# Performance work log

Hardware: AMD Instinct MI355X
Metric: run time of the kernel (lower is better)

Reference implementation:

```python
import jax, jax.numpy as jnp
import numpy as np

DIM = 96          # channels (= groups for depthwise conv)
NUM_EXPERTS = 6
TOP_K = 3
B, H, W = 8, 192, 192


def _dwconv(x, w, b):
    # depthwise 3x3, stride 1, pad 1, groups = DIM (flag == 'C' branch)
    y = jax.lax.conv_general_dilated(
        x, w, window_strides=(1, 1), padding=((1, 1), (1, 1)),
        feature_group_count=DIM,
        dimension_numbers=('NCHW', 'OIHW', 'NCHW'))
    return y + b[None, :, None, None]


def _expert(x, w1, b1, w2, b2):
    return _dwconv(jax.nn.relu(_dwconv(x, w1, b1)), w2, b2)


def _gate(x, w_fc0, b_fc0, w_fc1, b_fc1):
    # AdaptiveMaxPool2d(1) + AdaptiveAvgPool2d(1), then flatten -> (B, DIM)
    pooled = jnp.max(x, axis=(2, 3)) + jnp.mean(x, axis=(2, 3))
    g = jax.nn.leaky_relu(pooled @ w_fc1.T + b_fc1, negative_slope=0.2)
    noise = jax.nn.softplus(pooled @ w_fc0.T + b_fc0)
    mu = jnp.mean(noise, axis=1, keepdims=True)
    sd = jnp.std(noise, axis=1, keepdims=True, ddof=1)  # torch.std is unbiased
    scores = g + (noise - mu) / sd
    _, idx = jax.lax.top_k(scores, TOP_K)  # (B, K)
    mask = jnp.any(jax.nn.one_hot(idx, NUM_EXPERTS, dtype=jnp.float32) > 0, axis=1)  # (B, E)
    # non-top-k logits of g set to -inf, softmax over experts
    return jax.nn.softmax(jnp.where(mask, g, -jnp.inf), axis=1)


def setup_inputs() -> dict:
    key = jax.random.key(0)
    ks = jax.random.split(key, 9)
    s = 0.05
    return {
        'x': jax.random.normal(ks[0], (B, DIM, H, W), jnp.float32),
        'w_fc0': jax.random.normal(ks[1], (NUM_EXPERTS, DIM), jnp.float32) * s,
        'b_fc0': jax.random.normal(ks[2], (NUM_EXPERTS,), jnp.float32) * s,
        'w_fc1': jax.random.normal(ks[3], (NUM_EXPERTS, DIM), jnp.float32) * s,
        'b_fc1': jax.random.normal(ks[4], (NUM_EXPERTS,), jnp.float32) * s,
        'ew1': jax.random.normal(ks[5], (NUM_EXPERTS, DIM, 1, 3, 3), jnp.float32) * s,
        'eb1': jax.random.normal(ks[6], (NUM_EXPERTS, DIM), jnp.float32) * s,
        'ew2': jax.random.normal(ks[7], (NUM_EXPERTS, DIM, 1, 3, 3), jnp.float32) * s,
        'eb2': jax.random.normal(ks[8], (NUM_EXPERTS, DIM), jnp.float32) * s,
    }


def reference(x, w_fc0, b_fc0, w_fc1, b_fc1, ew1, eb1, ew2, eb2):
    cof = _gate(x, w_fc0, b_fc0, w_fc1, b_fc1)  # (B, E), zero for non-top-k
    # Dense dispatch: experts with cof==0 contribute nothing, matching the
    # torch masked gather/scatter-accumulate loop exactly.
    outs = jax.vmap(lambda w1, b1, w2, b2: _expert(x, w1, b1, w2, b2))(
        ew1, eb1, ew2, eb2)  # (E, B, C, H, W)
    return jnp.einsum('ebchw,be->bchw', outs, cof)
```

## Files before the change

### kernel.cpp

```cpp
#include <hip/hip_runtime.h>
#include <math.h>

#define DIM 96
#define NE 6
#define NB 8
#define H 192
#define W 192
#define HW (H * W)
#define NQ 4
#define QF4 (HW / 4 / NQ)

__global__ __launch_bounds__(256) void pool_partial(const float* __restrict__ x,
                                                    float* __restrict__ pmax,
                                                    float* __restrict__ psum) {
    int bc = blockIdx.x;
    int q = blockIdx.y;
    const float4* xp = (const float4*)(x + (size_t)bc * HW) + q * QF4;
    int tid = threadIdx.x;
    float vmax = -INFINITY, vsum = 0.f;
    for (int i = tid; i < QF4; i += 256) {
        float4 v = xp[i];
        vmax = fmaxf(vmax, fmaxf(fmaxf(v.x, v.y), fmaxf(v.z, v.w)));
        vsum += v.x + v.y + v.z + v.w;
    }
    for (int off = 32; off; off >>= 1) {
        vmax = fmaxf(vmax, __shfl_down(vmax, off, 64));
        vsum += __shfl_down(vsum, off, 64);
    }
    __shared__ float smax[4], ssum[4];
    if ((tid & 63) == 0) { smax[tid >> 6] = vmax; ssum[tid >> 6] = vsum; }
    __syncthreads();
    if (tid == 0) {
        float m = smax[0], s = ssum[0];
        for (int w = 1; w < 4; ++w) { m = fmaxf(m, smax[w]); s += ssum[w]; }
        pmax[q * (NB * DIM) + bc] = m;
        psum[q * (NB * DIM) + bc] = s;
    }
}

__global__ __launch_bounds__(128) void gate_kernel(const float* __restrict__ pmax,
                                                   const float* __restrict__ psum,
                                                   const float* __restrict__ w_fc0,
                                                   const float* __restrict__ b_fc0,
                                                   const float* __restrict__ w_fc1,
                                                   const float* __restrict__ b_fc1,
                                                   float* __restrict__ cof) {
    __shared__ float sp[NB * DIM];
    __shared__ float sw1[NE * DIM], sw0[NE * DIM];
    __shared__ float z1s[NB * NE], z0s[NB * NE];
    int tid = threadIdx.x;
    for (int i = tid; i < NB * DIM; i += 128) {
        float m = pmax[i], s = psum[i];
        for (int q = 1; q < NQ; ++q) {
            m = fmaxf(m, pmax[q * (NB * DIM) + i]);
            s += psum[q * (NB * DIM) + i];
        }
        sp[i] = m + s * (1.0f / (float)HW);
    }
    for (int i = tid; i < NE * DIM; i += 128) {
        sw1[i] = w_fc1[i];
        sw0[i] = w_fc0[i];
    }
    __syncthreads();
    if (tid < 2 * NB * NE) {
        int pair = (tid < NB * NE) ? tid : tid - NB * NE;
        int b = pair / NE, e = pair - b * NE;
        const float* wp = ((tid < NB * NE) ? sw1 : sw0) + e * DIM;
        float z = (tid < NB * NE) ? b_fc1[e] : b_fc0[e];
        const float* pp = sp + b * DIM;
        for (int i = 0; i < DIM; ++i) z = fmaf(pp[i], wp[i], z);
        if (tid < NB * NE) z1s[pair] = z; else z0s[pair] = z;
    }
    __syncthreads();
    if (tid < NB) {
        int b = tid;
        float g[NE], noise[NE];
        for (int e = 0; e < NE; ++e) {
            float z1 = z1s[b * NE + e], z0 = z0s[b * NE + e];
            g[e] = (z1 > 0.f) ? z1 : 0.2f * z1;
            noise[e] = (z0 > 20.f) ? z0 : log1pf(expf(z0));
        }
        float mu = 0.f;
        for (int e = 0; e < NE; ++e) mu += noise[e];
        mu *= (1.0f / NE);
        float var = 0.f;
        for (int e = 0; e < NE; ++e) { float d = noise[e] - mu; var += d * d; }
        var *= (1.0f / (NE - 1));
        float sd = sqrtf(var);
        float scores[NE];
        for (int e = 0; e < NE; ++e) scores[e] = g[e] + (noise[e] - mu) / sd;
        bool chosen[NE] = {false, false, false, false, false, false};
        for (int k = 0; k < 3; ++k) {
            float best = -INFINITY; int bi = 0;
            for (int e = 0; e < NE; ++e)
                if (!chosen[e] && scores[e] > best) { best = scores[e]; bi = e; }
            chosen[bi] = true;
        }
        float m = -INFINITY;
        for (int e = 0; e < NE; ++e) if (chosen[e]) m = fmaxf(m, g[e]);
        float s = 0.f;
        for (int e = 0; e < NE; ++e) if (chosen[e]) s += expf(g[e] - m);
        float inv = 1.0f / s;
        for (int e = 0; e < NE; ++e)
            cof[b * NE + e] = chosen[e] ? expf(g[e] - m) * inv : 0.f;
    }
}

#define TX 64
#define TY 32
#define IX (TX + 4)
#define IY (TY + 4)
#define YX (TX + 2)
#define YY (TY + 2)

__global__ __launch_bounds__(256) void moe_kernel(const float* __restrict__ x,
                                                  const float* __restrict__ ew1,
                                                  const float* __restrict__ eb1,
                                                  const float* __restrict__ ew2,
                                                  const float* __restrict__ eb2,
                                                  const float* __restrict__ cof,
                                                  float* __restrict__ out) {
    __shared__ float xs[IY][IX];
    __shared__ float ys[YY][YX];
    const int tile = blockIdx.x;
    const int c = blockIdx.y;
    const int b = blockIdx.z;
    const int tx0 = (tile % (W / TX)) * TX;
    const int ty0 = (tile / (W / TX)) * TY;
    const int tid = threadIdx.x;
    const int tx = tid & 63;
    const int wv = (tid >> 6) & 3;

    const float* xp = x + ((size_t)(b * DIM + c)) * HW;

    #pragma unroll
    for (int rr = 0; rr < 9; ++rr) {
        int r = wv + rr * 4;
        int gh = ty0 + r - 2;
        int gw = tx0 + tx - 2;
        float v = 0.f, v2 = 0.f;
        if (gh >= 0 && gh < H) {
            if (gw >= 0 && gw < W) v = xp[gh * W + gw];
            int gw2 = gw + 64;
            if (tx < 4 && gw2 < W) v2 = xp[gh * W + gw2];
        }
        xs[r][tx] = v;
        if (tx < 4) xs[r][tx + 64] = v2;
    }

    const bool topB = (ty0 == 0), botB = (ty0 == H - TY);
    const bool leftB = (tx0 == 0), rightB = (tx0 == W - TX);
    const int zr0 = topB ? 0 : -1;
    const int zr1 = botB ? (YY - 1) : -1;
    const bool lzero = leftB && (tx == 0);

    float acc[8];
    #pragma unroll
    for (int i = 0; i < 8; ++i) acc[i] = 0.f;

    const int rs = wv * 8 + (wv ? 1 : 0);
    const int r2 = wv * 8;

    for (int e = 0; e < NE; ++e) {
        float ce = cof[b * NE + e];
        if (ce == 0.f) continue;
        const float* w1 = ew1 + (size_t)(e * DIM + c) * 9;
        const float* w2 = ew2 + (size_t)(e * DIM + c) * 9;
        float w1r[9], w2r[9];
        #pragma unroll
        for (int k = 0; k < 9; ++k) { w1r[k] = w1[k]; w2r[k] = w2[k]; }
        const float bb1 = eb1[e * DIM + c];
        const float bb2 = eb2[e * DIM + c];

        __syncthreads();

        {
            float a0 = xs[rs][tx], a1 = xs[rs][tx + 1], a2 = xs[rs][tx + 2];
            float b0 = xs[rs + 1][tx], b1 = xs[rs + 1][tx + 1], b2 = xs[rs + 1][tx + 2];
            #pragma unroll
            for (int j = 0; j < 9; ++j) {
                int r = rs + j;
                float c0 = xs[r + 2][tx], c1 = xs[r + 2][tx + 1], c2 = xs[r + 2][tx + 2];
                float s = fmaf(w1r[0], a0, fmaf(w1r[1], a1, fmaf(w1r[2], a2, bb1)));
                s = fmaf(w1r[3], b0, fmaf(w1r[4], b1, fmaf(w1r[5], b2, s)));
                s = fmaf(w1r[6], c0, fmaf(w1r[7], c1, fmaf(w1r[8], c2, s)));
                float v = fmaxf(s, 0.f);
                if (r == zr0 || r == zr1 || lzero) v = 0.f;
                ys[r][tx] = v;
                a0 = b0; a1 = b1; a2 = b2;
                b0 = c0; b1 = c1; b2 = c2;
            }
        }
        if (tid < 2 * YY) {
            int r = tid >> 1;
            int cc = 64 + (tid & 1);
            float s = bb1;
            #pragma unroll
            for (int dr = 0; dr < 3; ++dr)
                #pragma unroll
                for (int dc = 0; dc < 3; ++dc)
                    s = fmaf(w1r[dr * 3 + dc], xs[r + dr][cc + dc], s);
            float v = fmaxf(s, 0.f);
            if (r == zr0 || r == zr1 || (rightB && cc == YX - 1)) v = 0.f;
            ys[r][cc] = v;
        }
        __syncthreads();

        {
            float p0 = ys[r2][tx], p1 = ys[r2][tx + 1], p2 = ys[r2][tx + 2];
            float q0 = ys[r2 + 1][tx], q1 = ys[r2 + 1][tx + 1], q2 = ys[r2 + 1][tx + 2];
            #pragma unroll
            for (int j = 0; j < 8; ++j) {
                float u0 = ys[r2 + j + 2][tx], u1 = ys[r2 + j + 2][tx + 1], u2 = ys[r2 + j + 2][tx + 2];
                float s = fmaf(w2r[0], p0, fmaf(w2r[1], p1, fmaf(w2r[2], p2, bb2)));
                s = fmaf(w2r[3], q0, fmaf(w2r[4], q1, fmaf(w2r[5], q2, s)));
                s = fmaf(w2r[6], u0, fmaf(w2r[7], u1, fmaf(w2r[8], u2, s)));
                acc[j] = fmaf(ce, s, acc[j]);
                p0 = q0; p1 = q1; p2 = q2;
                q0 = u0; q1 = u1; q2 = u2;
            }
        }
    }

    float* op = out + ((size_t)(b * DIM + c)) * HW + (size_t)(ty0 + r2) * W + tx0 + tx;
    #pragma unroll
    for (int j = 0; j < 8; ++j) op[j * W] = acc[j];
}

extern "C" void kernel_launch(void* const* d_in, const int* in_sizes, int n_in,
                              void* d_out, int out_size, void* d_ws, size_t ws_size,
                              hipStream_t stream) {
    const float* x     = (const float*)d_in[0];
    const float* w_fc0 = (const float*)d_in[1];
    const float* b_fc0 = (const float*)d_in[2];
    const float* w_fc1 = (const float*)d_in[3];
    const float* b_fc1 = (const float*)d_in[4];
    const float* ew1   = (const float*)d_in[5];
    const float* eb1   = (const float*)d_in[6];
    const float* ew2   = (const float*)d_in[7];
    const float* eb2   = (const float*)d_in[8];
    float* out = (float*)d_out;

    float* pmax = (float*)d_ws;
    float* psum = pmax + NQ * NB * DIM;
    float* cof  = psum + NQ * NB * DIM;

    dim3 pg(NB * DIM, NQ);
    pool_partial<<<pg, 256, 0, stream>>>(x, pmax, psum);
    gate_kernel<<<1, 128, 0, stream>>>(pmax, psum, w_fc0, b_fc0, w_fc1, b_fc1, cof);
    dim3 grid((W / TX) * (H / TY), DIM, NB);
    moe_kernel<<<grid, 256, 0, stream>>>(x, ew1, eb1, ew2, eb2, cof, out);
}
```

Before: 279.9 us.

## Restructure expert conv into full-width row strips with register-resident intermediates

The MoE kernel now has each block own a full-width 32-row strip. Each lane computes 3 adjacent columns and keeps the first conv's ReLU output in registers, trading neighbour values with wave shuffles instead of a shared-memory intermediate tile and its barriers. The three selected experts are found once up front, made wave-uniform with readfirstlane, and processed together per row, so the input is loaded into shared memory once with float4 reads. This removes repeated LDS round-trips and per-expert syncs and cuts halo recomputation, at the cost of much higher register pressure (weights for three experts plus rolling row buffers) and strided 3-element global stores.

```diff
diff --git a/kernel.cpp b/kernel.cpp
--- a/kernel.cpp
+++ b/kernel.cpp
@@ -106,12 +106,25 @@
     }
 }
 
-#define TX 64
 #define TY 32
-#define IX (TX + 4)
-#define IY (TY + 4)
-#define YX (TX + 2)
-#define YY (TY + 2)
+#define RPW 8
+#define SW 200
+#define XROWS (TY + 4)
+
+__device__ __forceinline__ float c3(const float* Wt, float bb,
+                                    const float* A, const float* B,
+                                    const float* Cc, int o) {
+    float s = fmaf(Wt[2], A[o + 2], bb);
+    s = fmaf(Wt[1], A[o + 1], s);
+    s = fmaf(Wt[0], A[o], s);
+    s = fmaf(Wt[5], B[o + 2], s);
+    s = fmaf(Wt[4], B[o + 1], s);
+    s = fmaf(Wt[3], B[o], s);
+    s = fmaf(Wt[8], Cc[o + 2], s);
+    s = fmaf(Wt[7], Cc[o + 1], s);
+    s = fmaf(Wt[6], Cc[o], s);
+    return s;
+}
 
 __global__ __launch_bounds__(256) void moe_kernel(const float* __restrict__ x,
                                                   const float* __restrict__ ew1,
@@ -120,111 +133,129 @@
                                                   const float* __restrict__ eb2,
                                                   const float* __restrict__ cof,
                                                   float* __restrict__ out) {
-    __shared__ float xs[IY][IX];
-    __shared__ float ys[YY][YX];
-    const int tile = blockIdx.x;
+    __shared__ float xs[XROWS * SW];
+    const int sb = blockIdx.x;
     const int c = blockIdx.y;
     const int b = blockIdx.z;
-    const int tx0 = (tile % (W / TX)) * TX;
-    const int ty0 = (tile / (W / TX)) * TY;
+    const int ty0 = sb * TY;
     const int tid = threadIdx.x;
-    const int tx = tid & 63;
-    const int wv = (tid >> 6) & 3;
+    const int lane = tid & 63;
+    const int wv = tid >> 6;
+
+    if (tid < 2 * XROWS) {
+        int r = tid >> 1;
+        int side = tid & 1;
+        *(float4*)&xs[r * SW + side * 196] = make_float4(0.f, 0.f, 0.f, 0.f);
+    }
 
     const float* xp = x + ((size_t)(b * DIM + c)) * HW;
-
-    #pragma unroll
-    for (int rr = 0; rr < 9; ++rr) {
-        int r = wv + rr * 4;
-        int gh = ty0 + r - 2;
-        int gw = tx0 + tx - 2;
-        float v = 0.f, v2 = 0.f;
-        if (gh >= 0 && gh < H) {
-            if (gw >= 0 && gw < W) v = xp[gh * W + gw];
-            int gw2 = gw + 64;
-            if (tx < 4 && gw2 < W) v2 = xp[gh * W + gw2];
-        }
-        xs[r][tx] = v;
-        if (tx < 4) xs[r][tx + 64] = v2;
-    }
-
-    const bool topB = (ty0 == 0), botB = (ty0 == H - TY);
-    const bool leftB = (tx0 == 0), rightB = (tx0 == W - TX);
-    const int zr0 = topB ? 0 : -1;
-    const int zr1 = botB ? (YY - 1) : -1;
-    const bool lzero = leftB && (tx == 0);
-
-    float acc[8];
-    #pragma unroll
-    for (int i = 0; i < 8; ++i) acc[i] = 0.f;
-
-    const int rs = wv * 8 + (wv ? 1 : 0);
-    const int r2 = wv * 8;
-
+    #pragma unroll
+    for (int it = 0; it < 7; ++it) {
+        int f = tid + it * 256;
+        if (f < XROWS * 48) {
+            int r = f / 48;
+            int k = f - r * 48;
+            int gh = ty0 + r - 2;
+            float4 v = make_float4(0.f, 0.f, 0.f, 0.f);
+            if (gh >= 0 && gh < H) v = *(const float4*)(xp + (size_t)gh * W + k * 4);
+            *(float4*)&xs[r * SW + 4 + k * 4] = v;
+        }
+    }
+
+    const float* cofb = cof + b * NE;
+    int e0 = 0, e1 = 0, e2 = 0;
+    float q0 = 0.f, q1 = 0.f, q2 = 0.f;
+    int n = 0;
+    #pragma unroll
     for (int e = 0; e < NE; ++e) {
-        float ce = cof[b * NE + e];
-        if (ce == 0.f) continue;
-        const float* w1 = ew1 + (size_t)(e * DIM + c) * 9;
-        const float* w2 = ew2 + (size_t)(e * DIM + c) * 9;
-        float w1r[9], w2r[9];
+        float ce = cofb[e];
+        if (ce != 0.f) {
+            if (n == 0)      { e0 = e; q0 = ce; }
+            else if (n == 1) { e1 = e; q1 = ce; }
+            else if (n == 2) { e2 = e; q2 = ce; }
+            ++n;
+        }
+    }
+    e0 = __builtin_amdgcn_readfirstlane(e0);
+    e1 = __builtin_amdgcn_readfirstlane(e1);
+    e2 = __builtin_amdgcn_readfirstlane(e2);
+    q0 = __int_as_float(__builtin_amdgcn_readfirstlane(__float_as_int(q0)));
+    q1 = __int_as_float(__builtin_amdgcn_readfirstlane(__float_as_int(q1)));
+    q2 = __int_as_float(__builtin_amdgcn_readfirstlane(__float_as_int(q2)));
+
+    const int eidx[3] = { e0, e1, e2 };
+    const float qv[3] = { q0, q1, q2 };
+    float W1[3][9], W2[3][9], B1[3], B2[3], CE[3];
+    #pragma unroll
+    for (int t = 0; t < 3; ++t) {
+        const int e = eidx[t];
+        const float* p1 = ew1 + (size_t)(e * DIM + c) * 9;
+        const float* p2 = ew2 + (size_t)(e * DIM + c) * 9;
         #pragma unroll
-        for (int k = 0; k < 9; ++k) { w1r[k] = w1[k]; w2r[k] = w2[k]; }
-        const float bb1 = eb1[e * DIM + c];
-        const float bb2 = eb2[e * DIM + c];
-
-        __syncthreads();
-
-        {
-            float a0 = xs[rs][tx], a1 = xs[rs][tx + 1], a2 = xs[rs][tx + 2];
-            float b0 = xs[rs + 1][tx], b1 = xs[rs + 1][tx + 1], b2 = xs[rs + 1][tx + 2];
-            #pragma unroll
-            for (int j = 0; j < 9; ++j) {
-                int r = rs + j;
-                float c0 = xs[r + 2][tx], c1 = xs[r + 2][tx + 1], c2 = xs[r + 2][tx + 2];
-                float s = fmaf(w1r[0], a0, fmaf(w1r[1], a1, fmaf(w1r[2], a2, bb1)));
-                s = fmaf(w1r[3], b0, fmaf(w1r[4], b1, fmaf(w1r[5], b2, s)));
-                s = fmaf(w1r[6], c0, fmaf(w1r[7], c1, fmaf(w1r[8], c2, s)));
-                float v = fmaxf(s, 0.f);
-                if (r == zr0 || r == zr1 || lzero) v = 0.f;
-                ys[r][tx] = v;
-                a0 = b0; a1 = b1; a2 = b2;
-                b0 = c0; b1 = c1; b2 = c2;
+        for (int k = 0; k < 9; ++k) { W1[t][k] = p1[k]; W2[t][k] = p2[k]; }
+        B1[t] = eb1[e * DIM + c];
+        B2[t] = eb2[e * DIM + c];
+        CE[t] = qv[t];
+    }
+
+    __syncthreads();
+
+    const int r0 = ty0 + wv * RPW;
+    const int lbase = (wv * RPW) * SW + 3 * lane + 3;
+    const bool l0 = (lane == 0);
+    const bool l63 = (lane == 63);
+
+    float X[3][5];
+    float Y[3][3][5];
+    #pragma unroll
+    for (int k = 0; k < 5; ++k) X[0][k] = xs[lbase + k];
+    #pragma unroll
+    for (int k = 0; k < 5; ++k) X[1][k] = xs[lbase + SW + k];
+
+    float* op = out + ((size_t)(b * DIM + c)) * HW + (size_t)r0 * W + 3 * lane;
+
+    #pragma unroll
+    for (int j = 0; j < RPW + 2; ++j) {
+        float* xN = X[(j + 2) % 3];
+        #pragma unroll
+        for (int k = 0; k < 5; ++k) xN[k] = xs[lbase + (j + 2) * SW + k];
+        const float* xA = X[j % 3];
+        const float* xB = X[(j + 1) % 3];
+        const float* xC = xN;
+        float a0 = 0.f, a1 = 0.f, a2 = 0.f;
+        #pragma unroll
+        for (int t = 0; t < 3; ++t) {
+            float y0 = c3(W1[t], B1[t], xA, xB, xC, 0);
+            float y1 = c3(W1[t], B1[t], xA, xB, xC, 1);
+            float y2 = c3(W1[t], B1[t], xA, xB, xC, 2);
+            y0 = fmaxf(y0, 0.f); y1 = fmaxf(y1, 0.f); y2 = fmaxf(y2, 0.f);
+            if (j == 0 || j == RPW + 1) {
+                int ry = r0 - 1 + j;
+                if (ry < 0 || ry >= H) { y0 = 0.f; y1 = 0.f; y2 = 0.f; }
             }
-        }
-        if (tid < 2 * YY) {
-            int r = tid >> 1;
-            int cc = 64 + (tid & 1);
-            float s = bb1;
-            #pragma unroll
-            for (int dr = 0; dr < 3; ++dr)
-                #pragma unroll
-                for (int dc = 0; dc < 3; ++dc)
-                    s = fmaf(w1r[dr * 3 + dc], xs[r + dr][cc + dc], s);
-            float v = fmaxf(s, 0.f);
-            if (r == zr0 || r == zr1 || (rightB && cc == YX - 1)) v = 0.f;
-            ys[r][cc] = v;
-        }
-        __syncthreads();
-
-        {
-            float p0 = ys[r2][tx], p1 = ys[r2][tx + 1], p2 = ys[r2][tx + 2];
-            float q0 = ys[r2 + 1][tx], q1 = ys[r2 + 1][tx + 1], q2 = ys[r2 + 1][tx + 2];
-            #pragma unroll
-            for (int j = 0; j < 8; ++j) {
-                float u0 = ys[r2 + j + 2][tx], u1 = ys[r2 + j + 2][tx + 1], u2 = ys[r2 + j + 2][tx + 2];
-                float s = fmaf(w2r[0], p0, fmaf(w2r[1], p1, fmaf(w2r[2], p2, bb2)));
-                s = fmaf(w2r[3], q0, fmaf(w2r[4], q1, fmaf(w2r[5], q2, s)));
-                s = fmaf(w2r[6], u0, fmaf(w2r[7], u1, fmaf(w2r[8], u2, s)));
-                acc[j] = fmaf(ce, s, acc[j]);
-                p0 = q0; p1 = q1; p2 = q2;
-                q0 = u0; q1 = u1; q2 = u2;
+            float yl = __shfl_up(y2, 1);
+            float yr = __shfl_down(y0, 1);
+            if (l0) yl = 0.f;
+            if (l63) yr = 0.f;
+            float* yw = Y[t][j % 3];
+            yw[0] = yl; yw[1] = y0; yw[2] = y1; yw[3] = y2; yw[4] = yr;
+            if (j >= 2) {
+                const float* pA = Y[t][(j + 1) % 3];
+                const float* pB = Y[t][(j + 2) % 3];
+                const float* pC = yw;
+                float s0 = c3(W2[t], B2[t], pA, pB, pC, 0);
+                float s1 = c3(W2[t], B2[t], pA, pB, pC, 1);
+                float s2 = c3(W2[t], B2[t], pA, pB, pC, 2);
+                a0 = fmaf(CE[t], s0, a0);
+                a1 = fmaf(CE[t], s1, a1);
+                a2 = fmaf(CE[t], s2, a2);
             }
         }
-    }
-
-    float* op = out + ((size_t)(b * DIM + c)) * HW + (size_t)(ty0 + r2) * W + tx0 + tx;
-    #pragma unroll
-    for (int j = 0; j < 8; ++j) op[j * W] = acc[j];
+        if (j >= 2) {
+            op[0] = a0; op[1] = a1; op[2] = a2;
+            op += W;
+        }
+    }
 }
 
 extern "C" void kernel_launch(void* const* d_in, const int* in_sizes, int n_in,
@@ -248,6 +279,6 @@
     dim3 pg(NB * DIM, NQ);
     pool_partial<<<pg, 256, 0, stream>>>(x, pmax, psum);
     gate_kernel<<<1, 128, 0, stream>>>(pmax, psum, w_fc0, b_fc0, w_fc1, b_fc1, cof);
-    dim3 grid((W / TX) * (H / TY), DIM, NB);
+    dim3 grid(H / TY, DIM, NB);
     moe_kernel<<<grid, 256, 0, stream>>>(x, ew1, eb1, ew2, eb2, cof, out);
 }
```

Result: faster. 266.7 us (-4.7%).
